# Performance work log

Measured on AMD Instinct MI355X. Metric: run time of the kernel, lower is better.

Reference implementation:

```python
import jax, jax.numpy as jnp
import numpy as np

FEATURE_DIM = 2048
CROP_PE_DIM = 96
FULL = FEATURE_DIM + CROP_PE_DIM  # 2144
H1 = 1024
H2 = 512
NEG_SLOPE = 0.01


def leaky(x):
    return jnp.where(x >= 0, x, NEG_SLOPE * x)


def setup_inputs() -> dict:
    key = jax.random.key(0)
    ks = jax.random.split(key, 8)
    B, T = 512, 32
    features = jax.random.normal(ks[0], (B, T, FULL), dtype=jnp.float32)

    def lin(k, fan_in, fan_out):
        kw, kb = jax.random.split(k)
        bound = 1.0 / np.sqrt(fan_in)
        W = jax.random.uniform(kw, (fan_in, fan_out), minval=-bound, maxval=bound, dtype=jnp.float32)
        b = jax.random.uniform(kb, (fan_out,), minval=-bound, maxval=bound, dtype=jnp.float32)
        return W, b

    We, be = lin(ks[1], 2 * FULL, H1)
    W1a, b1a = lin(ks[2], H1, H1)
    W1b, b1b = lin(ks[3], H1, H2)
    W2a, b2a = lin(ks[4], H2, H2)
    W2b, b2b = lin(ks[5], H2, H2)
    Wd, bd = lin(ks[6], H2, 3)
    return {
        "features": features,
        "We": We, "be": be,
        "W1a": W1a, "b1a": b1a, "W1b": W1b, "b1b": b1b,
        "W2a": W2a, "b2a": b2a, "W2b": W2b, "b2b": b2b,
        "Wd": Wd, "bd": bd,
    }


def reference(features, We, be, W1a, b1a, W1b, b1b, W2a, b2a, W2b, b2b, Wd, bd):
    B, T, D = features.shape
    # Vectorized version of the double Python loop: pair each token with token 0.
    anchor = jnp.broadcast_to(features[:, :1, :], (B, T, D))  # features[i][0]
    features_full = jnp.concatenate((features, anchor), axis=-1).reshape(B * T, 2 * D)
    e_f = features_full @ We + be
    h = leaky(leaky(e_f) @ W1a + b1a)
    h = h @ W1b + b1b  # block1 output
    h2 = leaky(leaky(h) @ W2a + b2a) @ W2b + b2b  # block2
    h = h + h2
    translations = leaky(h) @ Wd + bd  # (B*T, 3)
    bias = jnp.array([[0.0, 0.0, 1.0]], dtype=translations.dtype)
    return translations + bias
```

## Files before the change

### kernel.cpp

```cpp
#include <hip/hip_runtime.h>
#include <hip/hip_bf16.h>
#include <stdint.h>

typedef __attribute__((ext_vector_type(4))) float f32x4;
typedef __attribute__((ext_vector_type(8))) short bf16x8;

#define BK 64

__device__ inline void gload_lds16(const void* g, void* l) {
    __builtin_amdgcn_global_load_lds(
        (const __attribute__((address_space(1))) void*)g,
        (__attribute__((address_space(3))) void*)l, 16, 0, 0);
}

__device__ inline int xcd_swizzle(int orig, int nwg) {
    int q = nwg >> 3, r = nwg & 7;
    int xcd = orig & 7, idx = orig >> 3;
    int base = (xcd < r) ? xcd * (q + 1) : r * (q + 1) + (xcd - r) * q;
    return base + idx;
}

__device__ inline float b2f(short s) {
    union { float f; unsigned u; } x; x.u = ((unsigned)(unsigned short)s) << 16; return x.f;
}
__device__ inline short f2bs(float f) {
    __hip_bfloat16 h = __float2bfloat16(f);
    short s; __builtin_memcpy(&s, &h, 2); return s;
}

__global__ __launch_bounds__(256) void cvt_feat(const float* __restrict__ in,
                                                __hip_bfloat16* __restrict__ out) {
    int i = blockIdx.x * 256 + threadIdx.x;
    const int CH = 16384 * 272;
    if (i >= CH) return;
    int r = i / 272, c8 = (i % 272) * 8;
    __hip_bfloat16 tmp[8];
    if (c8 < 2144) {
        const float4* p = (const float4*)(in + (size_t)r * 2144 + c8);
        float4 x0 = p[0], x1 = p[1];
        tmp[0] = __float2bfloat16(x0.x); tmp[1] = __float2bfloat16(x0.y);
        tmp[2] = __float2bfloat16(x0.z); tmp[3] = __float2bfloat16(x0.w);
        tmp[4] = __float2bfloat16(x1.x); tmp[5] = __float2bfloat16(x1.y);
        tmp[6] = __float2bfloat16(x1.z); tmp[7] = __float2bfloat16(x1.w);
    } else {
        #pragma unroll
        for (int j = 0; j < 8; j++) tmp[j] = __float2bfloat16(0.f);
    }
    *(bf16x8*)&out[(size_t)r * 2176 + c8] = *(const bf16x8*)tmp;
}

__global__ __launch_bounds__(256) void cvt_wt_t(const float* __restrict__ W,
                                                __hip_bfloat16* __restrict__ WT,
                                                int K, int N, int KP) {
    __shared__ float tile[32][33];
    const int ntn = N >> 5;
    const int tk = blockIdx.x / ntn, tn = blockIdx.x - tk * ntn;
    const int k0 = tk * 32, n0 = tn * 32;
    const int c = threadIdx.x & 31, r8 = threadIdx.x >> 5;
    #pragma unroll
    for (int p = 0; p < 4; p++) {
        int k = k0 + r8 + p * 8;
        tile[r8 + p * 8][c] = (k < K) ? W[(size_t)k * N + n0 + c] : 0.f;
    }
    __syncthreads();
    #pragma unroll
    for (int p = 0; p < 4; p++) {
        int n = n0 + r8 + p * 8;
        WT[(size_t)n * KP + k0 + c] = __float2bfloat16(tile[c][r8 + p * 8]);
    }
}

template<int BN_, int RES_MODE, int OUTK>
__global__ __launch_bounds__(512, 2)
void gemm2ph(const __hip_bfloat16* __restrict__ A, int lda,
             const __hip_bfloat16* __restrict__ Bt,
             const float* __restrict__ bias,
             const __hip_bfloat16* __restrict__ resb,
             const float* __restrict__ resf,
             __hip_bfloat16* __restrict__ outb,
             __hip_bfloat16* __restrict__ outb2,
             float* __restrict__ outf,
             int M, int N, int K, int gx)
{
    constexpr int NF  = BN_ / 64;
    constexpr int REL = NF * 16;
    __shared__ __hip_bfloat16 lds[2][(256 + BN_) * BK];

    const int nwg  = gridDim.x;
    const int wgid = xcd_swizzle(blockIdx.x, nwg);
    const int by   = wgid / gx;
    const int bx   = wgid - by * gx;

    const int t    = threadIdx.x;
    const int lane = t & 63;
    const int wv   = t >> 6;
    const int wr   = wv >> 2;
    const int wc   = wv & 3;

    const int row0 = by * 256;
    const int col0 = bx * BN_;

    const int NT = K / BK;
    const int split = blockIdx.y;
    const int kb = (split * NT) / gridDim.y;
    const int ke = ((split + 1) * NT) / gridDim.y;
    float* outfs = outf;
    if (OUTK == 0 && gridDim.y > 1) outfs = outf + (size_t)split * M * N;

    const int srow = t >> 3;
    const int scol = ((t & 7) * 8) ^ ((srow & 7) << 3);
    const int sdst = (t & 7) * 8;

    f32x4 acc[8][NF];
    #pragma unroll
    for (int i = 0; i < 8; i++)
        #pragma unroll
        for (int j = 0; j < NF; j++)
            acc[i][j] = f32x4{0.f, 0.f, 0.f, 0.f};

    const int lrow = lane & 15;
    const int lk   = (lane >> 4) * 8;
    const int rxor = (lrow & 7) << 3;

    auto stage = [&](int buf, int kt) {
        const int k0 = kt * BK;
        #pragma unroll
        for (int r = 0; r < 4; ++r)
            gload_lds16(A + (size_t)(row0 + r * 64 + srow) * lda + k0 + scol,
                        &lds[buf][(r * 64 + srow) * BK + sdst]);
        #pragma unroll
        for (int r = 0; r < NF; ++r)
            gload_lds16(Bt + (size_t)(col0 + r * 64 + srow) * K + k0 + scol,
                        &lds[buf][(256 + r * 64 + srow) * BK + sdst]);
    };

    auto compute = [&](int buf) {
        __builtin_amdgcn_s_setprio(1);
        #pragma unroll
        for (int kk = 0; kk < BK; kk += 32) {
            const int kc = (kk + lk) ^ rxor;
            bf16x8 bg[NF];
            #pragma unroll
            for (int j = 0; j < NF; j++)
                bg[j] = *(const bf16x8*)&lds[buf][(256 + wc * REL + j * 16 + lrow) * BK + kc];
            #pragma unroll
            for (int i = 0; i < 8; i++) {
                bf16x8 af = *(const bf16x8*)&lds[buf][(wr * 128 + i * 16 + lrow) * BK + kc];
                #pragma unroll
                for (int j = 0; j < NF; j++)
                    acc[i][j] = __builtin_amdgcn_mfma_f32_16x16x32_bf16(af, bg[j], acc[i][j], 0, 0, 0);
            }
        }
        __builtin_amdgcn_s_setprio(0);
    };

    int cur = 0;
    stage(0, kb);
    for (int kt = kb; kt < ke - 1; ++kt) {
        stage(cur ^ 1, kt + 1);
        if constexpr (NF == 4) asm volatile("s_waitcnt vmcnt(8)" ::: "memory");
        else                   asm volatile("s_waitcnt vmcnt(6)" ::: "memory");
        __builtin_amdgcn_s_barrier();
        __builtin_amdgcn_sched_barrier(0);
        compute(cur);
        __builtin_amdgcn_s_barrier();
        cur ^= 1;
    }
    asm volatile("s_waitcnt vmcnt(0)" ::: "memory");
    __builtin_amdgcn_s_barrier();
    compute(cur);

    if constexpr (OUTK == 0) {
        #pragma unroll
        for (int j = 0; j < NF; j++) {
            const int col = col0 + wc * REL + j * 16 + lrow;
            #pragma unroll
            for (int i = 0; i < 8; i++) {
                const int rbase = row0 + wr * 128 + i * 16 + (lane >> 4) * 4;
                #pragma unroll
                for (int r = 0; r < 4; r++)
                    outfs[(size_t)(rbase + r) * N + col] = acc[i][j][r];
            }
        }
    } else {
        __builtin_amdgcn_s_barrier();
        __hip_bfloat16* eb = &lds[0][0] + wv * (128 * REL);
        #pragma unroll
        for (int i = 0; i < 8; i++)
            #pragma unroll
            for (int j = 0; j < NF; j++)
                #pragma unroll
                for (int r = 0; r < 4; r++)
                    eb[(i * 16 + (lane >> 4) * 4 + r) * REL + j * 16 + lrow] =
                        __float2bfloat16(acc[i][j][r]);
        constexpr int LPR = REL / 8;
        constexpr int RPI = 64 / LPR;
        constexpr int NIT = 128 / RPI;
        const int lrr = lane / LPR;
        const int lcc = (lane % LPR) * 8;
        const int col = col0 + wc * REL + lcc;
        float bvv[8];
        if (bias) {
            float4 b0 = *(const float4*)&bias[col];
            float4 b1 = *(const float4*)&bias[col + 4];
            bvv[0] = b0.x; bvv[1] = b0.y; bvv[2] = b0.z; bvv[3] = b0.w;
            bvv[4] = b1.x; bvv[5] = b1.y; bvv[6] = b1.z; bvv[7] = b1.w;
        } else {
            #pragma unroll
            for (int e = 0; e < 8; e++) bvv[e] = 0.f;
        }
        #pragma unroll
        for (int it = 0; it < NIT; it++) {
            const int rl  = it * RPI + lrr;
            const int row = row0 + wr * 128 + rl;
            bf16x8 v8 = *(bf16x8*)&eb[rl * REL + lcc];
            float vv[8];
            #pragma unroll
            for (int e = 0; e < 8; e++) vv[e] = b2f(v8[e]) + bvv[e];
            if constexpr (RES_MODE == 1) {
                bf16x8 r8 = *(const bf16x8*)&resb[(size_t)row * N + col];
                #pragma unroll
                for (int e = 0; e < 8; e++) vv[e] += b2f(r8[e]);
            }
            if constexpr (RES_MODE == 2) {
                const float* rp = &resf[(size_t)(row >> 5) * N + col];
                float4 r0 = *(const float4*)rp;
                float4 r1 = *(const float4*)(rp + 4);
                vv[0] += r0.x; vv[1] += r0.y; vv[2] += r0.z; vv[3] += r0.w;
                vv[4] += r1.x; vv[5] += r1.y; vv[6] += r1.z; vv[7] += r1.w;
            }
            bf16x8 o1, o2;
            #pragma unroll
            for (int e = 0; e < 8; e++) {
                float lv = vv[e] >= 0.f ? vv[e] : 0.01f * vv[e];
                if constexpr (OUTK == 1) o1[e] = f2bs(lv);
                if constexpr (OUTK == 2) o1[e] = f2bs(vv[e]);
                if constexpr (OUTK == 3) { o1[e] = f2bs(lv); o2[e] = f2bs(vv[e]); }
            }
            *(bf16x8*)&outb[(size_t)row * N + col] = o1;
            if constexpr (OUTK == 3)
                *(bf16x8*)&outb2[(size_t)row * N + col] = o2;
        }
    }
}

__global__ __launch_bounds__(256)
void anchor_reduce(const float* __restrict__ part, const float* __restrict__ be,
                   float* __restrict__ out) {
    int i = blockIdx.x * 256 + threadIdx.x;
    if (i >= 512 * 1024) return;
    const int S = 512 * 1024;
    int col = i & 1023;
    float s = be[col];
    #pragma unroll
    for (int p = 0; p < 8; p++) s += part[i + p * S];
    out[i] = s;
}

__global__ __launch_bounds__(256)
void final_head(const __hip_bfloat16* __restrict__ h, const float* __restrict__ Wd,
                const float* __restrict__ bd, float* __restrict__ out)
{
    int row  = blockIdx.x * 4 + (threadIdx.x >> 6);
    int lane = threadIdx.x & 63;
    const __hip_bfloat16* hr = h + (size_t)row * 512;
    bf16x8 v8 = *(const bf16x8*)&hr[lane * 8];
    float s0 = 0.f, s1 = 0.f, s2 = 0.f;
    #pragma unroll
    for (int e = 0; e < 8; e++) {
        float v = b2f(v8[e]);
        v = v >= 0.f ? v : 0.01f * v;
        int k = lane * 8 + e;
        s0 += v * Wd[k * 3 + 0];
        s1 += v * Wd[k * 3 + 1];
        s2 += v * Wd[k * 3 + 2];
    }
    #pragma unroll
    for (int off = 32; off > 0; off >>= 1) {
        s0 += __shfl_down(s0, off);
        s1 += __shfl_down(s1, off);
        s2 += __shfl_down(s2, off);
    }
    if (lane == 0) {
        out[row * 3 + 0] = s0 + bd[0];
        out[row * 3 + 1] = s1 + bd[1];
        out[row * 3 + 2] = s2 + bd[2] + 1.0f;
    }
}

extern "C" void kernel_launch(void* const* d_in, const int* in_sizes, int n_in,
                              void* d_out, int out_size, void* d_ws, size_t ws_size,
                              hipStream_t stream)
{
    const float* features = (const float*)d_in[0];
    const float* We  = (const float*)d_in[1];
    const float* be  = (const float*)d_in[2];
    const float* W1a = (const float*)d_in[3];
    const float* b1a = (const float*)d_in[4];
    const float* W1b = (const float*)d_in[5];
    const float* b1b = (const float*)d_in[6];
    const float* W2a = (const float*)d_in[7];
    const float* b2a = (const float*)d_in[8];
    const float* W2b = (const float*)d_in[9];
    const float* b2b = (const float*)d_in[10];
    const float* Wd  = (const float*)d_in[11];
    const float* bd  = (const float*)d_in[12];
    float* out = (float*)d_out;

    char* ws = (char*)d_ws;
    size_t off = 0;
    auto alloc = [&](size_t bytes) -> char* {
        char* p = ws + off;
        off += (bytes + 255) & ~(size_t)255;
        return p;
    };
    __hip_bfloat16* featbf = (__hip_bfloat16*)alloc(16384ull * 2176 * 2);
    __hip_bfloat16* WeTt   = (__hip_bfloat16*)alloc(1024ull * 2176 * 2);
    __hip_bfloat16* WeTb   = (__hip_bfloat16*)alloc(1024ull * 2176 * 2);
    __hip_bfloat16* W1aT   = (__hip_bfloat16*)alloc(1024ull * 1024 * 2);
    __hip_bfloat16* W1bT   = (__hip_bfloat16*)alloc(512ull * 1024 * 2);
    __hip_bfloat16* W2aT   = (__hip_bfloat16*)alloc(512ull * 512 * 2);
    __hip_bfloat16* W2bT   = (__hip_bfloat16*)alloc(512ull * 512 * 2);
    float* eanchor_part    = (float*)alloc(8ull * 512 * 1024 * 4);
    float* eanchor         = (float*)alloc(512ull * 1024 * 4);
    char* bufA             = alloc(16384ull * 1024 * 2);
    char* bufB             = alloc(16384ull * 1024 * 2);
    __hip_bfloat16* h1b    = (__hip_bfloat16*)alloc(16384ull * 512 * 2);

    __hip_bfloat16* act1   = (__hip_bfloat16*)bufA;
    __hip_bfloat16* act2   = (__hip_bfloat16*)bufB;
    __hip_bfloat16* act3   = (__hip_bfloat16*)bufA;
    __hip_bfloat16* act4   = (__hip_bfloat16*)bufB;
    __hip_bfloat16* hsum_b = (__hip_bfloat16*)bufA;

    cvt_feat<<<(16384 * 272 + 255) / 256, 256, 0, stream>>>(features, featbf);
    cvt_wt_t<<<68 * 32, 256, 0, stream>>>(We,               WeTt, 2144, 1024, 2176);
    cvt_wt_t<<<68 * 32, 256, 0, stream>>>(We + 2144 * 1024, WeTb, 2144, 1024, 2176);
    cvt_wt_t<<<32 * 32, 256, 0, stream>>>(W1a, W1aT, 1024, 1024, 1024);
    cvt_wt_t<<<32 * 16, 256, 0, stream>>>(W1b, W1bT, 1024, 512, 1024);
    cvt_wt_t<<<16 * 16, 256, 0, stream>>>(W2a, W2aT, 512, 512, 512);
    cvt_wt_t<<<16 * 16, 256, 0, stream>>>(W2b, W2bT, 512, 512, 512);

    gemm2ph<256, 0, 0><<<dim3(8, 8), 512, 0, stream>>>(
        featbf, 32 * 2176, WeTb, nullptr, nullptr, nullptr,
        nullptr, nullptr, eanchor_part, 512, 1024, 2176, 4);
    anchor_reduce<<<2048, 256, 0, stream>>>(eanchor_part, be, eanchor);

    gemm2ph<256, 2, 1><<<dim3(256), 512, 0, stream>>>(
        featbf, 2176, WeTt, nullptr, nullptr, eanchor,
        act1, nullptr, nullptr, 16384, 1024, 2176, 4);

    gemm2ph<256, 0, 1><<<dim3(256), 512, 0, stream>>>(
        act1, 1024, W1aT, b1a, nullptr, nullptr,
        act2, nullptr, nullptr, 16384, 1024, 1024, 4);

    gemm2ph<128, 0, 3><<<dim3(256), 512, 0, stream>>>(
        act2, 1024, W1bT, b1b, nullptr, nullptr,
        act3, h1b, nullptr, 16384, 512, 1024, 4);

    gemm2ph<128, 0, 1><<<dim3(256), 512, 0, stream>>>(
        act3, 512, W2aT, b2a, nullptr, nullptr,
        act4, nullptr, nullptr, 16384, 512, 512, 4);

    gemm2ph<128, 1, 2><<<dim3(256), 512, 0, stream>>>(
        act4, 512, W2bT, b2b, h1b, nullptr,
        hsum_b, nullptr, nullptr, 16384, 512, 512, 4);

    final_head<<<4096, 256, 0, stream>>>(hsum_b, Wd, bd, out);
}
```

Measured before the change: 256.2 us.

## Restructure GEMM main loop into eight-phase interleaved load/MFMA schedule

Replaces the two-phase stage/compute loop with a finer schedule that splits each K tile into quadrants of MFMAs. LDS fragment reads, global-to-LDS prefetch of individual row blocks, and barriers are interleaved between quadrants. The aim is to spread memory traffic across the compute phase and hide load latency better, in the style of HipKittens-like 8-wave ping-pong kernels. In exchange it adds more barriers per iteration and relies on hand-tuned vmcnt counts, which risks stalls or races if the counts are wrong.

```diff
diff --git a/kernel.cpp b/kernel.cpp
--- a/kernel.cpp
+++ b/kernel.cpp
@@ -12,6 +12,11 @@
         (const __attribute__((address_space(1))) void*)g,
         (__attribute__((address_space(3))) void*)l, 16, 0, 0);
 }
+
+__device__ inline void wg_barrier() {
+    asm volatile("s_barrier" ::: "memory");
+}
+#define SCHED0 __builtin_amdgcn_sched_barrier(0)
 
 __device__ inline int xcd_swizzle(int orig, int nwg) {
     int q = nwg >> 3, r = nwg & 7;
@@ -72,7 +77,7 @@
 
 template<int BN_, int RES_MODE, int OUTK>
 __global__ __launch_bounds__(512, 2)
-void gemm2ph(const __hip_bfloat16* __restrict__ A, int lda,
+void gemm8ph(const __hip_bfloat16* __restrict__ A, int lda,
              const __hip_bfloat16* __restrict__ Bt,
              const float* __restrict__ bias,
              const __hip_bfloat16* __restrict__ resb,
@@ -122,53 +127,110 @@
     const int lk   = (lane >> 4) * 8;
     const int rxor = (lrow & 7) << 3;
 
-    auto stage = [&](int buf, int kt) {
-        const int k0 = kt * BK;
-        #pragma unroll
-        for (int r = 0; r < 4; ++r)
-            gload_lds16(A + (size_t)(row0 + r * 64 + srow) * lda + k0 + scol,
-                        &lds[buf][(r * 64 + srow) * BK + sdst]);
-        #pragma unroll
-        for (int r = 0; r < NF; ++r)
-            gload_lds16(Bt + (size_t)(col0 + r * 64 + srow) * K + k0 + scol,
-                        &lds[buf][(256 + r * 64 + srow) * BK + sdst]);
+    auto stA = [&](int buf, int k0, int b) {
+        gload_lds16(A + (size_t)(row0 + b * 64 + srow) * lda + k0 + scol,
+                    &lds[buf][(b * 64 + srow) * BK + sdst]);
     };
-
-    auto compute = [&](int buf) {
-        __builtin_amdgcn_s_setprio(1);
-        #pragma unroll
-        for (int kk = 0; kk < BK; kk += 32) {
-            const int kc = (kk + lk) ^ rxor;
-            bf16x8 bg[NF];
-            #pragma unroll
-            for (int j = 0; j < NF; j++)
-                bg[j] = *(const bf16x8*)&lds[buf][(256 + wc * REL + j * 16 + lrow) * BK + kc];
-            #pragma unroll
-            for (int i = 0; i < 8; i++) {
-                bf16x8 af = *(const bf16x8*)&lds[buf][(wr * 128 + i * 16 + lrow) * BK + kc];
-                #pragma unroll
-                for (int j = 0; j < NF; j++)
-                    acc[i][j] = __builtin_amdgcn_mfma_f32_16x16x32_bf16(af, bg[j], acc[i][j], 0, 0, 0);
-            }
+    auto stB = [&](int buf, int k0, int b) {
+        gload_lds16(Bt + (size_t)(col0 + b * 64 + srow) * K + k0 + scol,
+                    &lds[buf][(256 + b * 64 + srow) * BK + sdst]);
+    };
+    auto rdA = [&](bf16x8 (&af)[4][2], int buf, int ih) {
+        #pragma unroll
+        for (int i = 0; i < 4; ++i)
+            #pragma unroll
+            for (int h = 0; h < 2; ++h)
+                af[i][h] = *(const bf16x8*)
+                    &lds[buf][(wr * 128 + (ih * 4 + i) * 16 + lrow) * BK + ((h * 32 + lk) ^ rxor)];
+    };
+    auto rdB = [&](bf16x8 (&bg)[2][2], int buf, int jb) {
+        #pragma unroll
+        for (int j = 0; j < 2; ++j)
+            #pragma unroll
+            for (int h = 0; h < 2; ++h)
+                bg[j][h] = *(const bf16x8*)
+                    &lds[buf][(256 + wc * REL + (jb + j) * 16 + lrow) * BK + ((h * 32 + lk) ^ rxor)];
+    };
+
+#define MFMA_Q(IB, JB)                                                        \
+    do {                                                                      \
+        __builtin_amdgcn_s_setprio(1);                                        \
+        _Pragma("unroll") for (int h_ = 0; h_ < 2; ++h_)                      \
+        _Pragma("unroll") for (int i_ = 0; i_ < 4; ++i_)                      \
+        _Pragma("unroll") for (int j_ = 0; j_ < 2; ++j_)                      \
+            acc[(IB) + i_][(JB) + j_] = __builtin_amdgcn_mfma_f32_16x16x32_bf16( \
+                af[i_][h_], bg[j_][h_], acc[(IB) + i_][(JB) + j_], 0, 0, 0);  \
+        __builtin_amdgcn_s_setprio(0);                                        \
+    } while (0)
+
+    {
+        const int k0 = kb * BK;
+        if constexpr (NF == 4) {
+            stA(0, k0, 0); stA(0, k0, 2);
+            stB(0, k0, 0); stB(0, k0, 1);
+            stB(0, k0, 2); stB(0, k0, 3);
+            stA(0, k0, 1); stA(0, k0, 3);
+        } else {
+            stA(0, k0, 0); stA(0, k0, 2);
+            stB(0, k0, 0); stB(0, k0, 1);
+            stA(0, k0, 1); stA(0, k0, 3);
         }
-        __builtin_amdgcn_s_setprio(0);
-    };
+    }
+    asm volatile("s_waitcnt vmcnt(2)" ::: "memory");
+    wg_barrier();
 
     int cur = 0;
-    stage(0, kb);
-    for (int kt = kb; kt < ke - 1; ++kt) {
-        stage(cur ^ 1, kt + 1);
-        if constexpr (NF == 4) asm volatile("s_waitcnt vmcnt(8)" ::: "memory");
-        else                   asm volatile("s_waitcnt vmcnt(6)" ::: "memory");
-        __builtin_amdgcn_s_barrier();
-        __builtin_amdgcn_sched_barrier(0);
-        compute(cur);
-        __builtin_amdgcn_s_barrier();
+    for (int kt = kb; kt < ke; ++kt) {
+        const bool pf = (kt + 1 < ke);
+        const int nk0 = (kt + 1) * BK;
+        bf16x8 af[4][2], bg[2][2];
+        if constexpr (NF == 4) {
+            rdA(af, cur, 0); rdB(bg, cur, 0);
+            if (pf) { stA(cur ^ 1, nk0, 0); stA(cur ^ 1, nk0, 2); }
+            wg_barrier(); SCHED0;
+            MFMA_Q(0, 0);
+            wg_barrier();
+            rdB(bg, cur, 2);
+            if (pf) { stB(cur ^ 1, nk0, 0); stB(cur ^ 1, nk0, 1); }
+            if (pf) asm volatile("s_waitcnt vmcnt(4)" ::: "memory");
+            else    asm volatile("s_waitcnt vmcnt(0)" ::: "memory");
+            wg_barrier(); SCHED0;
+            MFMA_Q(0, 2);
+            wg_barrier();
+            rdA(af, cur, 1); rdB(bg, cur, 0);
+            if (pf) { stB(cur ^ 1, nk0, 2); stB(cur ^ 1, nk0, 3); }
+            wg_barrier(); SCHED0;
+            MFMA_Q(4, 0);
+            wg_barrier();
+            rdB(bg, cur, 2);
+            if (pf) {
+                stA(cur ^ 1, nk0, 1); stA(cur ^ 1, nk0, 3);
+                asm volatile("s_waitcnt vmcnt(2)" ::: "memory");
+            }
+            wg_barrier(); SCHED0;
+            MFMA_Q(4, 2);
+            wg_barrier();
+        } else {
+            rdA(af, cur, 0); rdB(bg, cur, 0);
+            if (pf) { stA(cur ^ 1, nk0, 0); stA(cur ^ 1, nk0, 2);
+                      stB(cur ^ 1, nk0, 0); stB(cur ^ 1, nk0, 1); }
+            if (pf) asm volatile("s_waitcnt vmcnt(4)" ::: "memory");
+            else    asm volatile("s_waitcnt vmcnt(0)" ::: "memory");
+            wg_barrier(); SCHED0;
+            MFMA_Q(0, 0);
+            wg_barrier();
+            rdA(af, cur, 1);
+            if (pf) {
+                stA(cur ^ 1, nk0, 1); stA(cur ^ 1, nk0, 3);
+                asm volatile("s_waitcnt vmcnt(2)" ::: "memory");
+            }
+            wg_barrier(); SCHED0;
+            MFMA_Q(4, 0);
+            wg_barrier();
+        }
         cur ^= 1;
     }
-    asm volatile("s_waitcnt vmcnt(0)" ::: "memory");
-    __builtin_amdgcn_s_barrier();
-    compute(cur);
+#undef MFMA_Q
 
     if constexpr (OUTK == 0) {
         #pragma unroll
@@ -183,7 +245,7 @@
             }
         }
     } else {
-        __builtin_amdgcn_s_barrier();
+        wg_barrier();
         __hip_bfloat16* eb = &lds[0][0] + wv * (128 * REL);
         #pragma unroll
         for (int i = 0; i < 8; i++)
@@ -341,28 +403,28 @@
     cvt_wt_t<<<16 * 16, 256, 0, stream>>>(W2a, W2aT, 512, 512, 512);
     cvt_wt_t<<<16 * 16, 256, 0, stream>>>(W2b, W2bT, 512, 512, 512);
 
-    gemm2ph<256, 0, 0><<<dim3(8, 8), 512, 0, stream>>>(
+    gemm8ph<256, 0, 0><<<dim3(8, 8), 512, 0, stream>>>(
         featbf, 32 * 2176, WeTb, nullptr, nullptr, nullptr,
         nullptr, nullptr, eanchor_part, 512, 1024, 2176, 4);
     anchor_reduce<<<2048, 256, 0, stream>>>(eanchor_part, be, eanchor);
 
-    gemm2ph<256, 2, 1><<<dim3(256), 512, 0, stream>>>(
+    gemm8ph<256, 2, 1><<<dim3(256), 512, 0, stream>>>(
         featbf, 2176, WeTt, nullptr, nullptr, eanchor,
         act1, nullptr, nullptr, 16384, 1024, 2176, 4);
 
-    gemm2ph<256, 0, 1><<<dim3(256), 512, 0, stream>>>(
+    gemm8ph<256, 0, 1><<<dim3(256), 512, 0, stream>>>(
         act1, 1024, W1aT, b1a, nullptr, nullptr,
         act2, nullptr, nullptr, 16384, 1024, 1024, 4);
 
-    gemm2ph<128, 0, 3><<<dim3(256), 512, 0, stream>>>(
+    gemm8ph<128, 0, 3><<<dim3(256), 512, 0, stream>>>(
         act2, 1024, W1bT, b1b, nullptr, nullptr,
         act3, h1b, nullptr, 16384, 512, 1024, 4);
 
-    gemm2ph<128, 0, 1><<<dim3(256), 512, 0, stream>>>(
+    gemm8ph<128, 0, 1><<<dim3(256), 512, 0, stream>>>(
         act3, 512, W2aT, b2a, nullptr, nullptr,
         act4, nullptr, nullptr, 16384, 512, 512, 4);
 
-    gemm2ph<128, 1, 2><<<dim3(256), 512, 0, stream>>>(
+    gemm8ph<128, 1, 2><<<dim3(256), 512, 0, stream>>>(
         act4, 512, W2bT, b2b, h1b, nullptr,
         hsum_b, nullptr, nullptr, 16384, 512, 512, 4);
 
```

Result: no change. 257.0 us (+0.3%).
